# Kernel optimization log

Hardware: AMD Instinct MI355X
Metric: run time of the kernel (lower is better)

The kernel has to match this reference:

```python
import jax, jax.numpy as jnp
import numpy as np

N = 100000   # nodes
E = 1600000  # edges
D = 128      # feature dim
G = 64       # graphs in batch


def setup_inputs() -> dict:
    key = jax.random.key(0)
    k1, k2, k3, k4, k5, k6, k7, k8 = jax.random.split(key, 8)
    in_feat = jax.random.normal(k1, (N, D), dtype=jnp.float32)
    src = jax.random.randint(k2, (E,), 0, N, dtype=jnp.int32)
    dst = jax.random.randint(k3, (E,), 0, N, dtype=jnp.int32)
    graph_ids = jax.random.randint(k4, (N,), 0, G, dtype=jnp.int32)
    s = 1.0 / np.sqrt(D)
    W1 = jax.random.uniform(k5, (D, D), jnp.float32, -s, s)
    b1 = jnp.zeros((D,), jnp.float32)
    W2 = jax.random.uniform(k6, (D, D), jnp.float32, -s, s)
    b2 = jnp.zeros((D,), jnp.float32)
    return {"in_feat": in_feat, "W1": W1, "b1": b1, "W2": W2, "b2": b2,
            "src": src, "dst": dst, "graph_ids": graph_ids}


def _graph_conv(x, src, dst, W, b, norm_src, norm_dst):
    # DGL GraphConv, norm='both': D_out^{-1/2} A D_in^{-1/2} X W + b
    m = (x * norm_src[:, None])[src]                       # [E, d] gather
    agg = jax.ops.segment_sum(m, dst, num_segments=N)      # [N, d] scatter-add
    return (agg * norm_dst[:, None]) @ W + b


def reference(in_feat, W1, b1, W2, b2, src, dst, graph_ids):
    ones_e = jnp.ones((E,), jnp.float32)
    deg_out = jax.ops.segment_sum(ones_e, src, num_segments=N)
    deg_in = jax.ops.segment_sum(ones_e, dst, num_segments=N)
    norm_src = jnp.where(deg_out > 0, deg_out, 1.0) ** -0.5  # D_out^{-1/2}
    norm_dst = jnp.where(deg_in > 0, deg_in, 1.0) ** -0.5    # D_in^{-1/2}

    h = _graph_conv(in_feat, src, dst, W1, b1, norm_src, norm_dst)
    h = jax.nn.relu(h)
    h = _graph_conv(h, src, dst, W2, b2, norm_src, norm_dst)

    # AvgPooling: per-graph mean over nodes -> [G, D]
    sums = jax.ops.segment_sum(h, graph_ids, num_segments=G)
    counts = jax.ops.segment_sum(jnp.ones((N,), jnp.float32), graph_ids, num_segments=G)
    return sums / jnp.maximum(counts, 1.0)[:, None]
```

## Files before the change

### kernel.cpp

```cpp
#include <hip/hip_runtime.h>
#include <cstdint>


#define DD 128
#define PB 512
#define GB 384
#define KC 32
#define CHK 3200

typedef __attribute__((ext_vector_type(8))) short bf16x8;
typedef __attribute__((ext_vector_type(4))) float f32x4;
typedef __attribute__((ext_vector_type(2))) float f32x2;

__device__ __forceinline__ unsigned short f2bf(float f) {
  union { float f; unsigned u; } v; v.f = f;
  unsigned r = (v.u + 0x7fff + ((v.u >> 16) & 1)) >> 16;
  return (unsigned short)r;
}
__device__ __forceinline__ unsigned cvt_pk_bf16(float lo, float hi) {
  unsigned r;
  asm("v_cvt_pk_bf16_f32 %0, %1, %2" : "=v"(r) : "v"(lo), "v"(hi));
  return r;
}
__device__ __forceinline__ unsigned char f2fp8(float f) {
  return (unsigned char)(__builtin_amdgcn_cvt_pk_fp8_f32(f, f, 0, false) & 0xff);
}

__global__ __launch_bounds__(256) void k_part1a(const int* __restrict__ src, const int* __restrict__ dst,
                                                const int* __restrict__ gid,
                                                unsigned* __restrict__ rawD, unsigned* __restrict__ rawS,
                                                unsigned* __restrict__ tot,
                                                int* __restrict__ gcnt,
                                                const float* __restrict__ W1, unsigned short* __restrict__ Wt,
                                                unsigned char* __restrict__ zrow,
                                                int E, int N, int G) {
  if (blockIdx.x >= PB) {
    int wb = blockIdx.x - PB;
    int n = wb * 2 + (threadIdx.x >> 7), k = threadIdx.x & 127;
    Wt[n * 128 + k] = f2bf(W1[k * 128 + n]);
    if (wb == 0 && threadIdx.x < 128) zrow[threadIdx.x] = 0;
    return;
  }
  __shared__ unsigned hD[256], hS[256];
  __shared__ int h64[64];
  hD[threadIdx.x] = 0; hS[threadIdx.x] = 0;
  if (threadIdx.x < 64) h64[threadIdx.x] = 0;
  __syncthreads();
  int chunk = (E + PB - 1) / PB;
  int e0 = blockIdx.x * chunk, e1 = min(E, e0 + chunk);
  for (int e = e0 + threadIdx.x; e < e1; e += 256) {
    atomicAdd(&hD[(unsigned)dst[e] >> 9], 1u);
    atomicAdd(&hS[(unsigned)src[e] >> 9], 1u);
  }
  int stride = PB * 256;
  for (int i = blockIdx.x * 256 + threadIdx.x; i < N; i += stride)
    atomicAdd(&h64[gid[i]], 1);
  __syncthreads();
  unsigned vd = hD[threadIdx.x], vs = hS[threadIdx.x];
  rawD[blockIdx.x * 256 + threadIdx.x] = vd;
  rawS[blockIdx.x * 256 + threadIdx.x] = vs;
  if (vd) atomicAdd(&tot[threadIdx.x], vd);
  if (vs) atomicAdd(&tot[256 + threadIdx.x], vs);
  if (threadIdx.x < (unsigned)G) {
    int v = h64[threadIdx.x];
    if (v) atomicAdd(&gcnt[threadIdx.x], v);
  }
}

__global__ __launch_bounds__(256) void k_pscanB(const unsigned* __restrict__ tot,
                                                int* __restrict__ bsD, int* __restrict__ bsS,
                                                unsigned* __restrict__ curD, unsigned* __restrict__ curS) {
  __shared__ unsigned s[256];
  int t = threadIdx.x;
#pragma unroll
  for (int table = 0; table < 2; ++table) {
    int* bs = table ? bsS : bsD;
    unsigned* cur = table ? curS : curD;
    unsigned v = tot[table * 256 + t];
    s[t] = v;
    __syncthreads();
    for (int off = 1; off < 256; off <<= 1) {
      unsigned x = (t >= off) ? s[t - off] : 0;
      __syncthreads();
      s[t] += x;
      __syncthreads();
    }
    unsigned e = s[t] - v;
    bs[t] = (int)e;
    cur[t] = e;
    if (t == 255) bs[256] = (int)s[255];
    __syncthreads();
  }
}

__global__ __launch_bounds__(256) void k_part1c(const int* __restrict__ src, const int* __restrict__ dst,
                                                const unsigned* __restrict__ rawD, const unsigned* __restrict__ rawS,
                                                unsigned* __restrict__ curDg, unsigned* __restrict__ curSg,
                                                unsigned* __restrict__ pairD, unsigned* __restrict__ pairS, int E) {
  __shared__ unsigned pkD[CHK], pkS[CHK];
  __shared__ unsigned char bkD[CHK], bkS[CHK];
  __shared__ unsigned cD[256], cS[256], gbD[256], gbS[256], psc[256];
  int chunk = (E + gridDim.x - 1) / gridDim.x;
  int e0 = blockIdx.x * chunk, e1 = min(E, e0 + chunk);
  int n = e1 - e0;
  int t = threadIdx.x;
  unsigned vD = rawD[blockIdx.x * 256 + t];
  unsigned baseD = atomicAdd(&curDg[t], vD);
  psc[t] = vD;
  __syncthreads();
  for (int off = 1; off < 256; off <<= 1) {
    unsigned x = (t >= off) ? psc[t - off] : 0;
    __syncthreads();
    psc[t] += x;
    __syncthreads();
  }
  unsigned exD = psc[t] - vD;
  cD[t] = exD;
  gbD[t] = baseD - exD;
  __syncthreads();
  unsigned vS = rawS[blockIdx.x * 256 + t];
  unsigned baseS = atomicAdd(&curSg[t], vS);
  psc[t] = vS;
  __syncthreads();
  for (int off = 1; off < 256; off <<= 1) {
    unsigned x = (t >= off) ? psc[t - off] : 0;
    __syncthreads();
    psc[t] += x;
    __syncthreads();
  }
  unsigned exS = psc[t] - vS;
  cS[t] = exS;
  gbS[t] = baseS - exS;
  __syncthreads();
  for (int i = t; i < n; i += 256) {
    unsigned sv = (unsigned)src[e0 + i], dv = (unsigned)dst[e0 + i];
    unsigned bD = dv >> 9, bS = sv >> 9;
    unsigned pD = atomicAdd(&cD[bD], 1u);
    pkD[pD] = ((dv & 511u) << 17) | sv;
    bkD[pD] = (unsigned char)bD;
    unsigned pS = atomicAdd(&cS[bS], 1u);
    pkS[pS] = ((sv & 511u) << 17) | dv;
    bkS[pS] = (unsigned char)bS;
  }
  __syncthreads();
  for (int i = t; i < n; i += 256)
    pairD[gbD[bkD[i]] + i] = pkD[i];
  for (int i = t; i < n; i += 256)
    pairS[gbS[bkS[i]] + i] = pkS[i];
}

__global__ __launch_bounds__(256) void k_part2d(const unsigned* __restrict__ pairD, const int* __restrict__ bsD,
                                                const int* __restrict__ gcnt, const int* __restrict__ gid,
                                                int* __restrict__ offs, float* __restrict__ ndst,
                                                uint2* __restrict__ pwg, int* __restrict__ degI,
                                                int* __restrict__ dbin,
                                                int* __restrict__ srcS, int N) {
  __shared__ unsigned hist[512], excl[512], psc[256];
  __shared__ int ldb[256];
  int k = blockIdx.x, base = k << 9;
  int b0 = bsD[k], b1 = bsD[k + 1];
  hist[threadIdx.x] = 0; hist[threadIdx.x + 256] = 0;
  ldb[threadIdx.x] = 0;
  __syncthreads();
  for (int i = b0 + threadIdx.x; i < b1; i += 256)
    atomicAdd(&hist[pairD[i] >> 17], 1u);
  __syncthreads();
  unsigned s0 = hist[2 * threadIdx.x], s1 = hist[2 * threadIdx.x + 1];
  unsigned pr = s0 + s1;
  psc[threadIdx.x] = pr;
  __syncthreads();
  for (int off = 1; off < 256; off <<= 1) {
    unsigned x = (threadIdx.x >= off) ? psc[threadIdx.x - off] : 0;
    __syncthreads();
    psc[threadIdx.x] += x;
    __syncthreads();
  }
  unsigned pex = psc[threadIdx.x] - pr;
  excl[2 * threadIdx.x] = pex;
  excl[2 * threadIdx.x + 1] = pex + s0;
  __syncthreads();
  for (int j = threadIdx.x; j < 512; j += 256) {
    int node = base + j;
    if (node <= N) offs[node] = b0 + (int)excl[j];
    if (node < N) {
      int dg = (int)hist[j];
      degI[node] = dg;
      atomicAdd(&ldb[255 - min(dg, 255)], 1);
      float gi = (float)dg; gi = gi > 0.f ? gi : 1.f;
      float nd = rsqrtf(gi);
      ndst[node] = nd;
      float c = (float)gcnt[gid[node]]; c = c > 1.f ? c : 1.f;
      float w = nd / c;
      union { float f; unsigned u; } v; v.f = w;
      pwg[node] = make_uint2(v.u, (unsigned)gid[node]);
    }
  }
  __syncthreads();
  if (ldb[threadIdx.x]) atomicAdd(&dbin[threadIdx.x], ldb[threadIdx.x]);
  for (int i = b0 + threadIdx.x; i < b1; i += 256) {
    unsigned pkv = pairD[i];
    unsigned pos = atomicAdd(&excl[pkv >> 17], 1u);
    srcS[b0 + (int)pos] = (int)(pkv & 0x1FFFFu);
  }
}

__global__ __launch_bounds__(256) void k_dperm(const int* __restrict__ degI, const int* __restrict__ dbin,
                                               int* __restrict__ dcur,
                                               int* __restrict__ perm, int N) {
  __shared__ int s[256], lh[256], lcur[256];
  int t = threadIdx.x, i = blockIdx.x * 256 + t;
  int v = dbin[t];
  s[t] = v;
  lh[t] = 0;
  __syncthreads();
  for (int off = 1; off < 256; off <<= 1) {
    int x = (t >= off) ? s[t - off] : 0;
    __syncthreads();
    s[t] += x;
    __syncthreads();
  }
  int excl = s[t] - v;
  int bin = 0;
  if (i < N) {
    bin = 255 - min(degI[i], 255);
    atomicAdd(&lh[bin], 1);
  }
  __syncthreads();
  int r = lh[t] ? atomicAdd(&dcur[t], lh[t]) : 0;
  lcur[t] = excl + r;
  __syncthreads();
  if (i < N) {
    int pos = atomicAdd(&lcur[bin], 1);
    perm[pos] = i;
  }
}

__global__ __launch_bounds__(1024, 1) void k_pw(const unsigned* __restrict__ pairS, const int* __restrict__ bsS,
                                                const uint2* __restrict__ pwg,
                                                unsigned short* __restrict__ P16,
                                                float* __restrict__ nsrc, int N) {
  __shared__ float tile[512 * 64];
  __shared__ unsigned hist[512];
  int k = blockIdx.x, base = k << 9;
  int b0 = bsS[k], b1 = bsS[k + 1];
  for (int i = threadIdx.x; i < 512 * 64; i += 1024) tile[i] = 0.f;
  if (threadIdx.x < 512) hist[threadIdx.x] = 0;
  __syncthreads();
  for (int i = b0 + threadIdx.x; i < b1; i += 1024) {
    unsigned pkv = pairS[i];
    unsigned dv = pkv & 0x1FFFFu;
    unsigned sloc = pkv >> 17;
    atomicAdd(&hist[sloc], 1u);
    uint2 u = pwg[dv];
    union { unsigned u; float f; } w; w.u = u.x;
    atomicAdd(&tile[sloc * 64 + u.y], w.f);
  }
  __syncthreads();
  if (threadIdx.x < 512) {
    int node = base + threadIdx.x;
    if (node < N) {
      float g = (float)hist[threadIdx.x]; g = g > 0.f ? g : 1.f;
      nsrc[node] = rsqrtf(g);
    }
  }
  for (int grp = threadIdx.x; grp < 4096; grp += 1024) {
    int qb = grp >> 6, g = grp & 63;
    unsigned w0 = cvt_pk_bf16(tile[(qb * 8 + 0) * 64 + g], tile[(qb * 8 + 1) * 64 + g]);
    unsigned w1 = cvt_pk_bf16(tile[(qb * 8 + 2) * 64 + g], tile[(qb * 8 + 3) * 64 + g]);
    unsigned w2 = cvt_pk_bf16(tile[(qb * 8 + 4) * 64 + g], tile[(qb * 8 + 5) * 64 + g]);
    unsigned w3 = cvt_pk_bf16(tile[(qb * 8 + 6) * 64 + g], tile[(qb * 8 + 7) * 64 + g]);
    uint4 o = make_uint4(w0, w1, w2, w3);
    *(uint4*)(P16 + ((size_t)(base >> 3) + qb) * 512 + g * 8) = o;
  }
}

__global__ __launch_bounds__(512) void k_gemm1(const float* __restrict__ X, const unsigned short* __restrict__ Wt,
                                               const float* __restrict__ nsrc,
                                               unsigned char* __restrict__ Z8, int N) {
  __shared__ unsigned short Wl[128 * 128];
  int wave = threadIdx.x >> 6, lane = threadIdx.x & 63;
  int quad = lane >> 4, l16 = lane & 15;
  int row0 = blockIdx.x * 128 + wave * 16;
  int arow = row0 + l16; if (arow >= N) arow = N - 1;
  const float* xr = X + (size_t)arow * 128 + quad * 8;
  float4 xv[8];
#pragma unroll
  for (int kbi = 0; kbi < 4; ++kbi) {
    xv[2 * kbi]     = *(const float4*)(xr + kbi * 32);
    xv[2 * kbi + 1] = *(const float4*)(xr + kbi * 32 + 4);
  }
  int rbase = row0 + quad * 4;
  float sc[4];
#pragma unroll
  for (int r = 0; r < 4; ++r) {
    int row = rbase + r; if (row >= N) row = N - 1;
    sc[r] = nsrc[row];
  }
  for (int i = threadIdx.x; i < 2048; i += 512) {
    int wrow = i >> 4, sgrp = i & 15;
    *(uint4*)(Wl + wrow * 128 + ((sgrp ^ (wrow & 15)) << 3)) = ((const uint4*)Wt)[i];
  }
  __syncthreads();
  f32x4 acc[8];
#pragma unroll
  for (int i = 0; i < 8; ++i) acc[i] = (f32x4){0.f, 0.f, 0.f, 0.f};
#pragma unroll
  for (int kbi = 0; kbi < 4; ++kbi) {
    float4 x0 = xv[2 * kbi], x1 = xv[2 * kbi + 1];
    union { unsigned u[4]; bf16x8 v; } A;
    A.u[0] = cvt_pk_bf16(x0.x, x0.y);
    A.u[1] = cvt_pk_bf16(x0.z, x0.w);
    A.u[2] = cvt_pk_bf16(x1.x, x1.y);
    A.u[3] = cvt_pk_bf16(x1.z, x1.w);
#pragma unroll
    for (int nt = 0; nt < 8; ++nt) {
      bf16x8 b = *(const bf16x8*)(Wl + (nt * 16 + l16) * 128 + (((kbi * 4 + quad) ^ l16) << 3));
      acc[nt] = __builtin_amdgcn_mfma_f32_16x16x32_bf16(A.v, b, acc[nt], 0, 0, 0);
    }
  }
#pragma unroll
  for (int r = 0; r < 4; ++r) {
    int row = rbase + r;
    if (row < N) {
      float s = sc[r];
#pragma unroll
      for (int nt = 0; nt < 8; ++nt)
        Z8[(size_t)row * 128 + nt * 16 + l16] = f2fp8(acc[nt][r] * s);
    }
  }
}

#define ACC16(u) do {                                             \
    c0 += __builtin_amdgcn_cvt_pk_f32_fp8((u).x, false);          \
    c1 += __builtin_amdgcn_cvt_pk_f32_fp8((u).x, true);           \
    c2 += __builtin_amdgcn_cvt_pk_f32_fp8((u).y, false);          \
    c3 += __builtin_amdgcn_cvt_pk_f32_fp8((u).y, true);           \
    c4 += __builtin_amdgcn_cvt_pk_f32_fp8((u).z, false);          \
    c5 += __builtin_amdgcn_cvt_pk_f32_fp8((u).z, true);           \
    c6 += __builtin_amdgcn_cvt_pk_f32_fp8((u).w, false);          \
    c7 += __builtin_amdgcn_cvt_pk_f32_fp8((u).w, true);           \
  } while (0)

__global__ __launch_bounds__(256) void k_layer1(const unsigned char* __restrict__ Z8,
                                                const int* __restrict__ offs, const int* __restrict__ srcS,
                                                const int* __restrict__ perm,
                                                const float* __restrict__ b1,
                                                const float* __restrict__ nsrc, const float* __restrict__ ndst,
                                                unsigned short* __restrict__ Hb, int N) {
  int lane = threadIdx.x & 63;
  int oct = lane >> 3, l8 = lane & 7;
  const int f = l8 * 16;
  const unsigned char* zb = Z8 + f;
  int gstride = gridDim.x * 32;
  for (int base = blockIdx.x * 32; base < N; base += gstride) {
    int dd = base + (threadIdx.x >> 6) * 8 + oct;
    bool live = dd < N;
    int pd = perm[live ? dd : 0];
    int start = offs[pd];
    int end = live ? offs[pd + 1] : start;
    float nd = ndst[pd], ns = nsrc[pd];
    f32x2 c0 = {0.f, 0.f}, c1 = {0.f, 0.f}, c2 = {0.f, 0.f}, c3 = {0.f, 0.f};
    f32x2 c4 = {0.f, 0.f}, c5 = {0.f, 0.f}, c6 = {0.f, 0.f}, c7 = {0.f, 0.f};
    int e = start;
    int rem = end - start;
    int s0 = N, s1 = N, s2 = N, s3 = N;
    if (rem > 0) s0 = srcS[e];
    if (rem > 1) s1 = srcS[e + 1];
    if (rem > 2) s2 = srcS[e + 2];
    if (rem > 3) s3 = srcS[e + 3];
    while (__any(rem > 0)) {
      uint4 u0 = *(const uint4*)(zb + ((size_t)s0 << 7));
      uint4 u1 = *(const uint4*)(zb + ((size_t)s1 << 7));
      uint4 u2 = *(const uint4*)(zb + ((size_t)s2 << 7));
      uint4 u3 = *(const uint4*)(zb + ((size_t)s3 << 7));
      int n0 = N, n1 = N, n2 = N, n3 = N;
      if (rem > 4) n0 = srcS[e + 4];
      if (rem > 5) n1 = srcS[e + 5];
      if (rem > 6) n2 = srcS[e + 6];
      if (rem > 7) n3 = srcS[e + 7];
      ACC16(u0);
      ACC16(u1);
      ACC16(u2);
      ACC16(u3);
      s0 = n0; s1 = n1; s2 = n2; s3 = n3;
      e += 4;
      rem -= 4;
    }
    if (live) {
      float4 bv0 = *(const float4*)(b1 + f);
      float4 bv1 = *(const float4*)(b1 + f + 4);
      float4 bv2 = *(const float4*)(b1 + f + 8);
      float4 bv3 = *(const float4*)(b1 + f + 12);
      float h0 = fmaxf(fmaf(nd, c0[0], bv0.x), 0.f) * ns;
      float h1 = fmaxf(fmaf(nd, c0[1], bv0.y), 0.f) * ns;
      float h2 = fmaxf(fmaf(nd, c1[0], bv0.z), 0.f) * ns;
      float h3 = fmaxf(fmaf(nd, c1[1], bv0.w), 0.f) * ns;
      float h4 = fmaxf(fmaf(nd, c2[0], bv1.x), 0.f) * ns;
      float h5 = fmaxf(fmaf(nd, c2[1], bv1.y), 0.f) * ns;
      float h6 = fmaxf(fmaf(nd, c3[0], bv1.z), 0.f) * ns;
      float h7 = fmaxf(fmaf(nd, c3[1], bv1.w), 0.f) * ns;
      float h8 = fmaxf(fmaf(nd, c4[0], bv2.x), 0.f) * ns;
      float h9 = fmaxf(fmaf(nd, c4[1], bv2.y), 0.f) * ns;
      float hA = fmaxf(fmaf(nd, c5[0], bv2.z), 0.f) * ns;
      float hB = fmaxf(fmaf(nd, c5[1], bv2.w), 0.f) * ns;
      float hC = fmaxf(fmaf(nd, c6[0], bv3.x), 0.f) * ns;
      float hD = fmaxf(fmaf(nd, c6[1], bv3.y), 0.f) * ns;
      float hE = fmaxf(fmaf(nd, c7[0], bv3.z), 0.f) * ns;
      float hF = fmaxf(fmaf(nd, c7[1], bv3.w), 0.f) * ns;
      unsigned short* hrow = Hb + (size_t)pd * 128 + f;
      *(uint4*)hrow = make_uint4(cvt_pk_bf16(h0, h1), cvt_pk_bf16(h2, h3),
                                 cvt_pk_bf16(h4, h5), cvt_pk_bf16(h6, h7));
      *(uint4*)(hrow + 8) = make_uint4(cvt_pk_bf16(h8, h9), cvt_pk_bf16(hA, hB),
                                       cvt_pk_bf16(hC, hD), cvt_pk_bf16(hE, hF));
    }
  }
}

__global__ __launch_bounds__(256) void k_poolgemm(const unsigned short* __restrict__ P16,
                                                  const unsigned short* __restrict__ Hb,
                                                  float* __restrict__ pooled, int N, int Kpad, int chunk) {
  __shared__ unsigned short Hl[KC * 128];
  int t = threadIdx.x;
  int r0 = blockIdx.x * chunk;
  int r1 = min(Kpad, r0 + chunk);
  int wv = t >> 6, lane = t & 63, quad = lane >> 4, l16 = lane & 15;
  f32x4 acc[8];
#pragma unroll
  for (int i = 0; i < 8; ++i) acc[i] = (f32x4){0.f, 0.f, 0.f, 0.f};
  for (int rb = r0; rb < r1; rb += KC) {
    int r = t >> 3, c = (t & 7) * 16;
    int cs = c ^ ((r >> 3) * 16);
    int row = rb + r;
    if (row < N) {
      const uint4* srcp = (const uint4*)(Hb + (size_t)row * 128 + c);
      *(uint4*)(Hl + r * 128 + cs) = srcp[0];
      *(uint4*)(Hl + r * 128 + cs + 8) = srcp[1];
    } else {
      uint4 z = make_uint4(0, 0, 0, 0);
      *(uint4*)(Hl + r * 128 + cs) = z;
      *(uint4*)(Hl + r * 128 + cs + 8) = z;
    }
    __syncthreads();
    bf16x8 a = *(const bf16x8*)(P16 + ((size_t)(rb >> 3) + quad) * 512 + (wv * 16 + l16) * 8);
#pragma unroll
    for (int ft = 0; ft < 8; ++ft) {
      bf16x8 b;
#pragma unroll
      for (int j = 0; j < 8; ++j) {
        int rr = quad * 8 + j;
        b[j] = (short)Hl[rr * 128 + ((ft ^ (rr >> 3)) * 16) + l16];
      }
      acc[ft] = __builtin_amdgcn_mfma_f32_16x16x32_bf16(a, b, acc[ft], 0, 0, 0);
    }
    __syncthreads();
  }
#pragma unroll
  for (int ft = 0; ft < 8; ++ft)
#pragma unroll
    for (int rg = 0; rg < 4; ++rg)
      unsafeAtomicAdd(&pooled[(wv * 16 + quad * 4 + rg) * DD + ft * 16 + l16], acc[ft][rg]);
}

__global__ __launch_bounds__(128) void k_out(const float* __restrict__ pooled, const float* __restrict__ W2,
                                             const float* __restrict__ b2, float* __restrict__ out) {
  __shared__ float p[DD];
  int g = blockIdx.x, d = threadIdx.x;
  p[d] = pooled[g * DD + d];
  __syncthreads();
  float a = b2[d];
#pragma unroll 4
  for (int k = 0; k < DD; ++k) a = fmaf(p[k], W2[k * DD + d], a);
  out[g * DD + d] = a;
}

extern "C" void kernel_launch(void* const* d_in, const int* in_sizes, int n_in,
                              void* d_out, int out_size, void* d_ws, size_t ws_size,
                              hipStream_t stream) {
  const float* X  = (const float*)d_in[0];
  const float* W1 = (const float*)d_in[1];
  const float* b1 = (const float*)d_in[2];
  const float* W2 = (const float*)d_in[3];
  const float* b2 = (const float*)d_in[4];
  const int* src  = (const int*)d_in[5];
  const int* dst  = (const int*)d_in[6];
  const int* gid  = (const int*)d_in[7];
  int E = in_sizes[5];
  int N = in_sizes[7];
  int G = out_size / DD;
  int nb = (N >> 9) + 1;
  int Kpad = nb << 9;
  int chunk = ((Kpad + GB * KC - 1) / (GB * KC)) * KC;

  char* w = (char*)d_ws;
  size_t o = 0;
  auto carve = [&](size_t bytes) { char* p = w + o; o += (bytes + 255) & ~(size_t)255; return p; };
  int*   gcnt   = (int*)  carve((size_t)G * 4);
  float* pooled = (float*)carve((size_t)G * DD * 4);
  int*   dbin   = (int*)  carve(256 * 4);
  unsigned* tot = (unsigned*)carve(512 * 4);
  int*   dcur   = (int*)  carve(256 * 4);
  size_t zeroBytes = o;
  unsigned* rawD  = (unsigned*)carve((size_t)PB * 256 * 4);
  unsigned* rawS  = (unsigned*)carve((size_t)PB * 256 * 4);
  int*   bsD    = (int*)  carve(257 * 4);
  int*   bsS    = (int*)  carve(257 * 4);
  unsigned* curD = (unsigned*)carve(256 * 4);
  unsigned* curS = (unsigned*)carve(256 * 4);
  unsigned* pairD = (unsigned*)carve((size_t)E * 4);
  unsigned* pairS = (unsigned*)carve((size_t)E * 4);
  int*   srcS   = (int*)  carve((size_t)E * 4);
  int*   offs   = (int*)  carve((size_t)(N + 1) * 4);
  int*   degI   = (int*)  carve((size_t)N * 4);
  int*   perm   = (int*)  carve((size_t)N * 4);
  float* nsrc   = (float*)carve((size_t)N * 4);
  float* ndst   = (float*)carve((size_t)N * 4);
  uint2* pwg    = (uint2*)carve((size_t)N * 8);
  unsigned short* Wt = (unsigned short*)carve(128 * 128 * 2);
  unsigned char*  Z8 = (unsigned char*)carve((size_t)(N + 1) * DD);
  unsigned short* Hb = (unsigned short*)carve((size_t)N * DD * 2);
  unsigned short* P16 = (unsigned short*)carve((size_t)Kpad * 64 * 2);

  hipMemsetAsync(d_ws, 0, zeroBytes, stream);

  k_part1a<<<PB + 64, 256, 0, stream>>>(src, dst, gid, rawD, rawS, tot, gcnt,
                                        W1, Wt, Z8 + (size_t)N * DD, E, N, G);
  k_pscanB<<<1, 256, 0, stream>>>(tot, bsD, bsS, curD, curS);
  k_part1c<<<PB, 256, 0, stream>>>(src, dst, rawD, rawS, curD, curS, pairD, pairS, E);
  k_part2d<<<nb, 256, 0, stream>>>(pairD, bsD, gcnt, gid, offs, ndst, pwg, degI, dbin, srcS, N);
  k_dperm<<<(N + 255) / 256, 256, 0, stream>>>(degI, dbin, dcur, perm, N);
  k_pw<<<nb, 1024, 0, stream>>>(pairS, bsS, pwg, P16, nsrc, N);
  k_gemm1<<<(N + 127) / 128, 512, 0, stream>>>(X, Wt, nsrc, Z8, N);
  k_layer1<<<1024, 256, 0, stream>>>(Z8, offs, srcS, perm, b1, nsrc, ndst, Hb, N);
  k_poolgemm<<<GB, 256, 0, stream>>>(P16, Hb, pooled, N, Kpad, chunk);
  k_out<<<G, DD, 0, stream>>>(pooled, W2, b2, (float*)d_out);
}
```

Measured before the change: 275.9 us.

## Fold bucket scan into consumers and merge degree-permutation into pw kernel

Removes the single-block k_pscanB launch by having k_part1c, k_part2d and k_pw each recompute the 256-entry bucket prefix scan from the totals. The cur counters become zero-initialised offsets relative to each bucket base. k_dperm is folded into k_pw as extra 1024-thread blocks, cutting two kernel launches and their serialisation gaps. In exchange, every block repeats a small scan, and the perm blocks run with much larger thread blocks.

```diff
diff --git a/kernel.cpp b/kernel.cpp
--- a/kernel.cpp
+++ b/kernel.cpp
@@ -67,34 +67,9 @@
   }
 }
 
-__global__ __launch_bounds__(256) void k_pscanB(const unsigned* __restrict__ tot,
-                                                int* __restrict__ bsD, int* __restrict__ bsS,
-                                                unsigned* __restrict__ curD, unsigned* __restrict__ curS) {
-  __shared__ unsigned s[256];
-  int t = threadIdx.x;
-#pragma unroll
-  for (int table = 0; table < 2; ++table) {
-    int* bs = table ? bsS : bsD;
-    unsigned* cur = table ? curS : curD;
-    unsigned v = tot[table * 256 + t];
-    s[t] = v;
-    __syncthreads();
-    for (int off = 1; off < 256; off <<= 1) {
-      unsigned x = (t >= off) ? s[t - off] : 0;
-      __syncthreads();
-      s[t] += x;
-      __syncthreads();
-    }
-    unsigned e = s[t] - v;
-    bs[t] = (int)e;
-    cur[t] = e;
-    if (t == 255) bs[256] = (int)s[255];
-    __syncthreads();
-  }
-}
-
 __global__ __launch_bounds__(256) void k_part1c(const int* __restrict__ src, const int* __restrict__ dst,
                                                 const unsigned* __restrict__ rawD, const unsigned* __restrict__ rawS,
+                                                const unsigned* __restrict__ tot,
                                                 unsigned* __restrict__ curDg, unsigned* __restrict__ curSg,
                                                 unsigned* __restrict__ pairD, unsigned* __restrict__ pairS, int E) {
   __shared__ unsigned pkD[CHK], pkS[CHK];
@@ -105,7 +80,18 @@
   int n = e1 - e0;
   int t = threadIdx.x;
   unsigned vD = rawD[blockIdx.x * 256 + t];
+  unsigned tD = tot[t];
   unsigned baseD = atomicAdd(&curDg[t], vD);
+  psc[t] = tD;
+  __syncthreads();
+  for (int off = 1; off < 256; off <<= 1) {
+    unsigned x = (t >= off) ? psc[t - off] : 0;
+    __syncthreads();
+    psc[t] += x;
+    __syncthreads();
+  }
+  unsigned bsDt = psc[t] - tD;
+  __syncthreads();
   psc[t] = vD;
   __syncthreads();
   for (int off = 1; off < 256; off <<= 1) {
@@ -116,10 +102,21 @@
   }
   unsigned exD = psc[t] - vD;
   cD[t] = exD;
-  gbD[t] = baseD - exD;
+  gbD[t] = bsDt + baseD - exD;
   __syncthreads();
   unsigned vS = rawS[blockIdx.x * 256 + t];
+  unsigned tS = tot[256 + t];
   unsigned baseS = atomicAdd(&curSg[t], vS);
+  psc[t] = tS;
+  __syncthreads();
+  for (int off = 1; off < 256; off <<= 1) {
+    unsigned x = (t >= off) ? psc[t - off] : 0;
+    __syncthreads();
+    psc[t] += x;
+    __syncthreads();
+  }
+  unsigned bsSt = psc[t] - tS;
+  __syncthreads();
   psc[t] = vS;
   __syncthreads();
   for (int off = 1; off < 256; off <<= 1) {
@@ -130,7 +127,7 @@
   }
   unsigned exS = psc[t] - vS;
   cS[t] = exS;
-  gbS[t] = baseS - exS;
+  gbS[t] = bsSt + baseS - exS;
   __syncthreads();
   for (int i = t; i < n; i += 256) {
     unsigned sv = (unsigned)src[e0 + i], dv = (unsigned)dst[e0 + i];
@@ -149,37 +146,47 @@
     pairS[gbS[bkS[i]] + i] = pkS[i];
 }
 
-__global__ __launch_bounds__(256) void k_part2d(const unsigned* __restrict__ pairD, const int* __restrict__ bsD,
+__global__ __launch_bounds__(256) void k_part2d(const unsigned* __restrict__ pairD,
+                                                const unsigned* __restrict__ tot,
                                                 const int* __restrict__ gcnt, const int* __restrict__ gid,
                                                 int* __restrict__ offs, float* __restrict__ ndst,
                                                 uint2* __restrict__ pwg, int* __restrict__ degI,
                                                 int* __restrict__ dbin,
                                                 int* __restrict__ srcS, int N) {
   __shared__ unsigned hist[512], excl[512], psc[256];
-  __shared__ int ldb[256];
+  __shared__ int sInc[256], ldb[256];
   int k = blockIdx.x, base = k << 9;
-  int b0 = bsD[k], b1 = bsD[k + 1];
-  hist[threadIdx.x] = 0; hist[threadIdx.x + 256] = 0;
-  ldb[threadIdx.x] = 0;
-  __syncthreads();
-  for (int i = b0 + threadIdx.x; i < b1; i += 256)
+  int t = threadIdx.x;
+  sInc[t] = (int)tot[t];
+  hist[t] = 0; hist[t + 256] = 0;
+  ldb[t] = 0;
+  __syncthreads();
+  for (int off = 1; off < 256; off <<= 1) {
+    int x = (t >= off) ? sInc[t - off] : 0;
+    __syncthreads();
+    sInc[t] += x;
+    __syncthreads();
+  }
+  int b0 = k ? sInc[k - 1] : 0;
+  int b1 = sInc[k];
+  for (int i = b0 + t; i < b1; i += 256)
     atomicAdd(&hist[pairD[i] >> 17], 1u);
   __syncthreads();
-  unsigned s0 = hist[2 * threadIdx.x], s1 = hist[2 * threadIdx.x + 1];
+  unsigned s0 = hist[2 * t], s1 = hist[2 * t + 1];
   unsigned pr = s0 + s1;
-  psc[threadIdx.x] = pr;
-  __syncthreads();
-  for (int off = 1; off < 256; off <<= 1) {
-    unsigned x = (threadIdx.x >= off) ? psc[threadIdx.x - off] : 0;
-    __syncthreads();
-    psc[threadIdx.x] += x;
-    __syncthreads();
-  }
-  unsigned pex = psc[threadIdx.x] - pr;
-  excl[2 * threadIdx.x] = pex;
-  excl[2 * threadIdx.x + 1] = pex + s0;
-  __syncthreads();
-  for (int j = threadIdx.x; j < 512; j += 256) {
+  psc[t] = pr;
+  __syncthreads();
+  for (int off = 1; off < 256; off <<= 1) {
+    unsigned x = (t >= off) ? psc[t - off] : 0;
+    __syncthreads();
+    psc[t] += x;
+    __syncthreads();
+  }
+  unsigned pex = psc[t] - pr;
+  excl[2 * t] = pex;
+  excl[2 * t + 1] = pex + s0;
+  __syncthreads();
+  for (int j = t; j < 512; j += 256) {
     int node = base + j;
     if (node <= N) offs[node] = b0 + (int)excl[j];
     if (node < N) {
@@ -196,57 +203,69 @@
     }
   }
   __syncthreads();
-  if (ldb[threadIdx.x]) atomicAdd(&dbin[threadIdx.x], ldb[threadIdx.x]);
-  for (int i = b0 + threadIdx.x; i < b1; i += 256) {
+  if (ldb[t]) atomicAdd(&dbin[t], ldb[t]);
+  for (int i = b0 + t; i < b1; i += 256) {
     unsigned pkv = pairD[i];
     unsigned pos = atomicAdd(&excl[pkv >> 17], 1u);
     srcS[b0 + (int)pos] = (int)(pkv & 0x1FFFFu);
   }
 }
 
-__global__ __launch_bounds__(256) void k_dperm(const int* __restrict__ degI, const int* __restrict__ dbin,
-                                               int* __restrict__ dcur,
-                                               int* __restrict__ perm, int N) {
-  __shared__ int s[256], lh[256], lcur[256];
-  int t = threadIdx.x, i = blockIdx.x * 256 + t;
-  int v = dbin[t];
-  s[t] = v;
-  lh[t] = 0;
-  __syncthreads();
-  for (int off = 1; off < 256; off <<= 1) {
-    int x = (t >= off) ? s[t - off] : 0;
-    __syncthreads();
-    s[t] += x;
-    __syncthreads();
-  }
-  int excl = s[t] - v;
-  int bin = 0;
-  if (i < N) {
-    bin = 255 - min(degI[i], 255);
-    atomicAdd(&lh[bin], 1);
-  }
-  __syncthreads();
-  int r = lh[t] ? atomicAdd(&dcur[t], lh[t]) : 0;
-  lcur[t] = excl + r;
-  __syncthreads();
-  if (i < N) {
-    int pos = atomicAdd(&lcur[bin], 1);
-    perm[pos] = i;
-  }
-}
-
-__global__ __launch_bounds__(1024, 1) void k_pw(const unsigned* __restrict__ pairS, const int* __restrict__ bsS,
+__global__ __launch_bounds__(1024, 1) void k_pw(const unsigned* __restrict__ pairS,
+                                                const unsigned* __restrict__ tot,
                                                 const uint2* __restrict__ pwg,
                                                 unsigned short* __restrict__ P16,
-                                                float* __restrict__ nsrc, int N) {
+                                                float* __restrict__ nsrc,
+                                                const int* __restrict__ degI, const int* __restrict__ dbin,
+                                                int* __restrict__ dcur, int* __restrict__ perm,
+                                                int N, int nbk) {
   __shared__ float tile[512 * 64];
   __shared__ unsigned hist[512];
+  __shared__ int s2[256], lh[256], lcur[256];
+  int t = threadIdx.x;
+  if (blockIdx.x >= nbk) {
+    int v2 = 0;
+    if (t < 256) { s2[t] = dbin[t]; v2 = s2[t]; lh[t] = 0; }
+    __syncthreads();
+    for (int off = 1; off < 256; off <<= 1) {
+      int x = (t < 256 && t >= off) ? s2[t - off] : 0;
+      __syncthreads();
+      if (t < 256) s2[t] += x;
+      __syncthreads();
+    }
+    int i = (blockIdx.x - nbk) * 1024 + t;
+    int bin = 0;
+    if (i < N) {
+      bin = 255 - min(degI[i], 255);
+      atomicAdd(&lh[bin], 1);
+    }
+    __syncthreads();
+    if (t < 256) {
+      int r = lh[t] ? atomicAdd(&dcur[t], lh[t]) : 0;
+      lcur[t] = (s2[t] - v2) + r;
+    }
+    __syncthreads();
+    if (i < N) {
+      int pos = atomicAdd(&lcur[bin], 1);
+      perm[pos] = i;
+    }
+    return;
+  }
   int k = blockIdx.x, base = k << 9;
-  int b0 = bsS[k], b1 = bsS[k + 1];
-  for (int i = threadIdx.x; i < 512 * 64; i += 1024) tile[i] = 0.f;
-  if (threadIdx.x < 512) hist[threadIdx.x] = 0;
-  __syncthreads();
-  for (int i = b0 + threadIdx.x; i < b1; i += 1024) {
+  if (t < 256) s2[t] = (int)tot[256 + t];
+  __syncthreads();
+  for (int off = 1; off < 256; off <<= 1) {
+    int x = (t < 256 && t >= off) ? s2[t - off] : 0;
+    __syncthreads();
+    if (t < 256) s2[t] += x;
+    __syncthreads();
+  }
+  int b0 = k ? s2[k - 1] : 0;
+  int b1 = s2[k];
+  for (int i = t; i < 512 * 64; i += 1024) tile[i] = 0.f;
+  if (t < 512) hist[t] = 0;
+  __syncthreads();
+  for (int i = b0 + t; i < b1; i += 1024) {
     unsigned pkv = pairS[i];
     unsigned dv = pkv & 0x1FFFFu;
     unsigned sloc = pkv >> 17;
@@ -256,14 +275,14 @@
     atomicAdd(&tile[sloc * 64 + u.y], w.f);
   }
   __syncthreads();
-  if (threadIdx.x < 512) {
-    int node = base + threadIdx.x;
+  if (t < 512) {
+    int node = base + t;
     if (node < N) {
-      float g = (float)hist[threadIdx.x]; g = g > 0.f ? g : 1.f;
+      float g = (float)hist[t]; g = g > 0.f ? g : 1.f;
       nsrc[node] = rsqrtf(g);
     }
   }
-  for (int grp = threadIdx.x; grp < 4096; grp += 1024) {
+  for (int grp = t; grp < 4096; grp += 1024) {
     int qb = grp >> 6, g = grp & 63;
     unsigned w0 = cvt_pk_bf16(tile[(qb * 8 + 0) * 64 + g], tile[(qb * 8 + 1) * 64 + g]);
     unsigned w1 = cvt_pk_bf16(tile[(qb * 8 + 2) * 64 + g], tile[(qb * 8 + 3) * 64 + g]);
@@ -490,6 +509,7 @@
   int nb = (N >> 9) + 1;
   int Kpad = nb << 9;
   int chunk = ((Kpad + GB * KC - 1) / (GB * KC)) * KC;
+  int ndb = (N + 1023) / 1024;
 
   char* w = (char*)d_ws;
   size_t o = 0;
@@ -499,13 +519,11 @@
   int*   dbin   = (int*)  carve(256 * 4);
   unsigned* tot = (unsigned*)carve(512 * 4);
   int*   dcur   = (int*)  carve(256 * 4);
+  unsigned* curD = (unsigned*)carve(256 * 4);
+  unsigned* curS = (unsigned*)carve(256 * 4);
   size_t zeroBytes = o;
   unsigned* rawD  = (unsigned*)carve((size_t)PB * 256 * 4);
   unsigned* rawS  = (unsigned*)carve((size_t)PB * 256 * 4);
-  int*   bsD    = (int*)  carve(257 * 4);
-  int*   bsS    = (int*)  carve(257 * 4);
-  unsigned* curD = (unsigned*)carve(256 * 4);
-  unsigned* curS = (unsigned*)carve(256 * 4);
   unsigned* pairD = (unsigned*)carve((size_t)E * 4);
   unsigned* pairS = (unsigned*)carve((size_t)E * 4);
   int*   srcS   = (int*)  carve((size_t)E * 4);
@@ -524,11 +542,9 @@
 
   k_part1a<<<PB + 64, 256, 0, stream>>>(src, dst, gid, rawD, rawS, tot, gcnt,
                                         W1, Wt, Z8 + (size_t)N * DD, E, N, G);
-  k_pscanB<<<1, 256, 0, stream>>>(tot, bsD, bsS, curD, curS);
-  k_part1c<<<PB, 256, 0, stream>>>(src, dst, rawD, rawS, curD, curS, pairD, pairS, E);
-  k_part2d<<<nb, 256, 0, stream>>>(pairD, bsD, gcnt, gid, offs, ndst, pwg, degI, dbin, srcS, N);
-  k_dperm<<<(N + 255) / 256, 256, 0, stream>>>(degI, dbin, dcur, perm, N);
-  k_pw<<<nb, 1024, 0, stream>>>(pairS, bsS, pwg, P16, nsrc, N);
+  k_part1c<<<PB, 256, 0, stream>>>(src, dst, rawD, rawS, tot, curD, curS, pairD, pairS, E);
+  k_part2d<<<nb, 256, 0, stream>>>(pairD, tot, gcnt, gid, offs, ndst, pwg, degI, dbin, srcS, N);
+  k_pw<<<nb + ndb, 1024, 0, stream>>>(pairS, tot, pwg, P16, nsrc, degI, dbin, dcur, perm, N, nb);
   k_gemm1<<<(N + 127) / 128, 512, 0, stream>>>(X, Wt, nsrc, Z8, N);
   k_layer1<<<1024, 256, 0, stream>>>(Z8, offs, srcS, perm, b1, nsrc, ndst, Hb, N);
   k_poolgemm<<<GB, 256, 0, stream>>>(P16, Hb, pooled, N, Kpad, chunk);
```

Measured after the change: 270.0 us (median of 3 runs). 1.02x faster.
